# Performance work log

Measured on AMD Instinct MI355X. Metric: run time of the kernel, lower is better.

Reference implementation:

```python
import jax, jax.numpy as jnp
import numpy as np

N_NODES = 100000
N_EDGES = 1600000
NFEAT = 512
HIDDEN = 128
NCLASS = 40


def setup_inputs() -> dict:
    key = jax.random.key(0)
    ks = jax.random.split(key, 8)
    x = jax.random.normal(ks[0], (N_NODES, NFEAT), dtype=jnp.float32)
    edge_src = jax.random.randint(ks[1], (N_EDGES,), 0, N_NODES, dtype=jnp.int32)
    edge_dst = jax.random.randint(ks[2], (N_EDGES,), 0, N_NODES, dtype=jnp.int32)
    # normalized adjacency values (D^-1/2 A D^-1/2 style), all positive
    edge_val = jax.random.uniform(ks[3], (N_EDGES,), dtype=jnp.float32)
    # glorot-ish init like pygcn's reset_parameters
    W1 = jax.random.normal(ks[4], (NFEAT, HIDDEN), dtype=jnp.float32) / np.sqrt(NFEAT)
    b1 = jnp.zeros((HIDDEN,), dtype=jnp.float32)
    W2 = jax.random.normal(ks[5], (HIDDEN, NCLASS), dtype=jnp.float32) / np.sqrt(HIDDEN)
    b2 = jnp.zeros((NCLASS,), dtype=jnp.float32)
    return {"x": x, "edge_src": edge_src, "edge_dst": edge_dst, "edge_val": edge_val,
            "W1": W1, "b1": b1, "W2": W2, "b2": b2}


def _gcn_layer(h, edge_src, edge_dst, edge_val, W, b):
    # support = h @ W ; out = spmm(adj, support) + b
    support = h @ W                                  # [N, d_out]
    msg = support[edge_src] * edge_val[:, None]      # [E, d_out] gather
    agg = jax.ops.segment_sum(msg, edge_dst, num_segments=N_NODES)  # scatter-add
    return agg + b


def reference(x, edge_src, edge_dst, edge_val, W1, b1, W2, b2):
    h = _gcn_layer(x, edge_src, edge_dst, edge_val, W1, b1)
    h = jax.nn.relu(h)
    # dropout=0.0 -> branch skipped (faithful to `if self.dropout:` with falsy value)
    h = _gcn_layer(h, edge_src, edge_dst, edge_val, W2, b2)
    return jax.nn.log_softmax(h, axis=1)
```

## Files before the change

kernel.cpp:

```cpp
#include <hip/hip_runtime.h>
#include <stdint.h>

#define NN 100000
#define NE 1600000
#define NF 512
#define NH 128
#define NC 40
#define BKT 64
#define DEGS 16
#define NGB 782

typedef float f32x4 __attribute__((ext_vector_type(4)));
typedef short bf16x8 __attribute__((ext_vector_type(8)));

__device__ __forceinline__ unsigned short f2bf(float f){
    unsigned u = __float_as_uint(f);
    u = u + 0x7FFFu + ((u >> 16) & 1u);
    return (unsigned short)(u >> 16);
}
__device__ __forceinline__ unsigned pk2(float a, float b){
    return (unsigned)f2bf(a) | ((unsigned)f2bf(b) << 16);
}
__device__ __forceinline__ float blo(unsigned u){ return __uint_as_float(u << 16); }
__device__ __forceinline__ float bhi(unsigned u){ return __uint_as_float(u & 0xffff0000u); }

__global__ __launch_bounds__(256) void wprep(const float* __restrict__ W1, const float* __restrict__ W2,
                                             unsigned short* __restrict__ W1t, unsigned short* __restrict__ W2t){
    int tid = blockIdx.x * 256 + threadIdx.x;
    if (tid < NF * NH){
        int c = tid >> 9;
        int k = tid & 511;
        W1t[c * NF + k] = f2bf(W1[k * NH + c]);
    }
    int t2 = tid - NF * NH;
    if (t2 >= 0 && t2 < 48 * NH){
        int c = t2 >> 7;
        int k = t2 & 127;
        W2t[c * NH + k] = (c < NC) ? f2bf(W2[k * NC + c]) : (unsigned short)0;
    }
}

__global__ __launch_bounds__(256, 3) void gemm1_edge(const float* __restrict__ x,
                                                     const unsigned short* __restrict__ W1t,
                                                     unsigned short* __restrict__ s1,
                                                     const int* __restrict__ esrc,
                                                     const int* __restrict__ edst,
                                                     const float* __restrict__ eval,
                                                     int* __restrict__ deg, int2* __restrict__ pk){
    __shared__ unsigned short Al[2][128 * 40];
    __shared__ unsigned short Bl[2][128 * 40];
    if (blockIdx.x >= NGB){
        int tid = (blockIdx.x - NGB) * 256 + threadIdx.x;
        if (tid < NE){
            int d = edst[tid];
            int pos = atomicAdd(&deg[d * DEGS], 1);
            if (pos < BKT)
                pk[(size_t)d * BKT + pos] = make_int2(esrc[tid], __float_as_int(eval[tid]));
        }
        return;
    }
    const int tid  = threadIdx.x;
    const int wid  = tid >> 6;
    const int lane = tid & 63;
    const int quad = lane >> 4;
    const int l15  = lane & 15;
    const int br   = blockIdx.x * 128;

    const int r    = tid >> 1;
    const int half = tid & 1;

    int arow = br + r; if (arow >= NN) arow = NN - 1;
    const float* aptr = x + (size_t)arow * NF + half * 16;
    const unsigned short* bptr = W1t + (size_t)r * NF + half * 16;

    float4 pa0, pa1, pa2, pa3;
    uint4  pb0, pb1;
    {
        const float4* ap = (const float4*)aptr;
        pa0 = ap[0]; pa1 = ap[1]; pa2 = ap[2]; pa3 = ap[3];
        const uint4* bp = (const uint4*)bptr;
        pb0 = bp[0]; pb1 = bp[1];
        unsigned* Ad = (unsigned*)&Al[0][r * 40 + half * 16];
        Ad[0] = pk2(pa0.x, pa0.y); Ad[1] = pk2(pa0.z, pa0.w);
        Ad[2] = pk2(pa1.x, pa1.y); Ad[3] = pk2(pa1.z, pa1.w);
        Ad[4] = pk2(pa2.x, pa2.y); Ad[5] = pk2(pa2.z, pa2.w);
        Ad[6] = pk2(pa3.x, pa3.y); Ad[7] = pk2(pa3.z, pa3.w);
        uint4* Bd = (uint4*)&Bl[0][r * 40 + half * 16];
        Bd[0] = pb0; Bd[1] = pb1;
    }
    __syncthreads();

    f32x4 acc[2][8];
#pragma unroll
    for (int i = 0; i < 2; i++)
#pragma unroll
        for (int j = 0; j < 8; j++) acc[i][j] = (f32x4){0.f, 0.f, 0.f, 0.f};

    int cur = 0;
    for (int ks = 0; ks < NF; ks += 32){
        const bool more = (ks + 32 < NF);
        if (more){
            const float4* ap = (const float4*)(aptr + ks + 32);
            pa0 = ap[0]; pa1 = ap[1]; pa2 = ap[2]; pa3 = ap[3];
            const uint4* bp = (const uint4*)(bptr + ks + 32);
            pb0 = bp[0]; pb1 = bp[1];
        }

        bf16x8 a0 = *(const bf16x8*)&Al[cur][(wid * 32 +      l15) * 40 + quad * 8];
        bf16x8 a1 = *(const bf16x8*)&Al[cur][(wid * 32 + 16 + l15) * 40 + quad * 8];
        bf16x8 bb[8];
#pragma unroll
        for (int ct = 0; ct < 8; ct++)
            bb[ct] = *(const bf16x8*)&Bl[cur][(ct * 16 + l15) * 40 + quad * 8];
#pragma unroll
        for (int ct = 0; ct < 8; ct++){
            acc[0][ct] = __builtin_amdgcn_mfma_f32_16x16x32_bf16(a0, bb[ct], acc[0][ct], 0, 0, 0);
            acc[1][ct] = __builtin_amdgcn_mfma_f32_16x16x32_bf16(a1, bb[ct], acc[1][ct], 0, 0, 0);
        }

        if (more){
            int nxt = cur ^ 1;
            unsigned* Ad = (unsigned*)&Al[nxt][r * 40 + half * 16];
            Ad[0] = pk2(pa0.x, pa0.y); Ad[1] = pk2(pa0.z, pa0.w);
            Ad[2] = pk2(pa1.x, pa1.y); Ad[3] = pk2(pa1.z, pa1.w);
            Ad[4] = pk2(pa2.x, pa2.y); Ad[5] = pk2(pa2.z, pa2.w);
            Ad[6] = pk2(pa3.x, pa3.y); Ad[7] = pk2(pa3.z, pa3.w);
            uint4* Bd = (uint4*)&Bl[nxt][r * 40 + half * 16];
            Bd[0] = pb0; Bd[1] = pb1;
        }
        __syncthreads();
        cur ^= 1;
    }

#pragma unroll
    for (int rt = 0; rt < 2; rt++)
#pragma unroll
        for (int ct = 0; ct < 8; ct++)
#pragma unroll
            for (int i = 0; i < 4; i++){
                int row = br + wid * 32 + rt * 16 + quad * 4 + i;
                if (row < NN) s1[(size_t)row * NH + ct * 16 + l15] = f2bf(acc[rt][ct][i]);
            }
}

__global__ __launch_bounds__(256) void agg1g2(const uint4* __restrict__ s1v,
                                              const int* __restrict__ deg,
                                              const int2* __restrict__ pk,
                                              const float* __restrict__ b1,
                                              const unsigned short* __restrict__ W2t,
                                              unsigned short* __restrict__ s2p){
    __shared__ unsigned short Hl[64][136];
    const int tid   = threadIdx.x;
    const int wid   = tid >> 6;
    const int lane  = tid & 63;
    const int quad  = lane >> 4;
    const int hl    = lane & 15;
    const int lbase = quad * 16;
    const int nb    = blockIdx.x * 64;

    const float4* b1v = (const float4*)b1;
    const float4 bA = b1v[2 * hl], bB = b1v[2 * hl + 1];

#pragma unroll
    for (int pass = 0; pass < 4; pass++){
        const int nloc = pass * 16 + wid * 4 + quad;
        const int node = nb + nloc;
        float a[8];
#pragma unroll
        for (int t = 0; t < 8; t++) a[t] = 0.f;

        if (node < NN){
            const int s = node * BKT;
            int dg = deg[node * DEGS]; if (dg > BKT) dg = BKT;
            const int e = s + dg;

            int2 rec = make_int2(0, 0);
            {
                int c0 = e - s; if (c0 > 16) c0 = 16;
                if (hl < c0) rec = pk[s + hl];
            }
            for (int base = s; base < e; base += 16){
                int cnt = e - base; if (cnt > 16) cnt = 16;
                int2 cur = rec;
                int nxb = base + 16;
                if (nxb < e){
                    int cn = e - nxb; if (cn > 16) cn = 16;
                    rec = make_int2(0, 0);
                    if (hl < cn) rec = pk[nxb + hl];
                }
                int j = 0;
                for (; j + 8 <= cnt; j += 8){
                    int is[8];
#pragma unroll
                    for (int q = 0; q < 8; q++) is[q] = __shfl(cur.x, lbase + j + q, 64);
                    uint4 us[8];
#pragma unroll
                    for (int q = 0; q < 8; q++) us[q] = s1v[(size_t)is[q] * 16 + hl];
                    float vs[8];
#pragma unroll
                    for (int q = 0; q < 8; q++) vs[q] = __int_as_float(__shfl(cur.y, lbase + j + q, 64));
#pragma unroll
                    for (int q = 0; q < 8; q++){
                        float v = vs[q];
                        a[0] += v * blo(us[q].x); a[1] += v * bhi(us[q].x);
                        a[2] += v * blo(us[q].y); a[3] += v * bhi(us[q].y);
                        a[4] += v * blo(us[q].z); a[5] += v * bhi(us[q].z);
                        a[6] += v * blo(us[q].w); a[7] += v * bhi(us[q].w);
                    }
                }
                for (; j < cnt; j++){
                    int   i0 = __shfl(cur.x, lbase + j, 64);
                    float v0 = __int_as_float(__shfl(cur.y, lbase + j, 64));
                    uint4 u  = s1v[(size_t)i0 * 16 + hl];
                    a[0] += v0 * blo(u.x); a[1] += v0 * bhi(u.x);
                    a[2] += v0 * blo(u.y); a[3] += v0 * bhi(u.y);
                    a[4] += v0 * blo(u.z); a[5] += v0 * bhi(u.z);
                    a[6] += v0 * blo(u.w); a[7] += v0 * bhi(u.w);
                }
            }
            a[0] += bA.x; a[1] += bA.y; a[2] += bA.z; a[3] += bA.w;
            a[4] += bB.x; a[5] += bB.y; a[6] += bB.z; a[7] += bB.w;
#pragma unroll
            for (int t = 0; t < 8; t++) a[t] = fmaxf(a[t], 0.f);
        }
        *(uint4*)&Hl[nloc][hl * 8] = make_uint4(pk2(a[0], a[1]), pk2(a[2], a[3]),
                                                pk2(a[4], a[5]), pk2(a[6], a[7]));
    }
    __syncthreads();

    bf16x8 bf[3][4];
#pragma unroll
    for (int ct = 0; ct < 3; ct++)
#pragma unroll
        for (int ks = 0; ks < 4; ks++)
            bf[ct][ks] = *(const bf16x8*)&W2t[(ct * 16 + hl) * NH + ks * 32 + quad * 8];

    bf16x8 af[4];
#pragma unroll
    for (int ks = 0; ks < 4; ks++)
        af[ks] = *(const bf16x8*)&Hl[wid * 16 + hl][ks * 32 + quad * 8];

    f32x4 acc[3];
#pragma unroll
    for (int ct = 0; ct < 3; ct++) acc[ct] = (f32x4){0.f, 0.f, 0.f, 0.f};
#pragma unroll
    for (int ks = 0; ks < 4; ks++)
#pragma unroll
        for (int ct = 0; ct < 3; ct++)
            acc[ct] = __builtin_amdgcn_mfma_f32_16x16x32_bf16(af[ks], bf[ct][ks], acc[ct], 0, 0, 0);

#pragma unroll
    for (int ct = 0; ct < 3; ct++)
#pragma unroll
        for (int i = 0; i < 4; i++){
            int row = nb + wid * 16 + quad * 4 + i;
            if (row < NN) s2p[(size_t)row * 64 + ct * 16 + hl] = f2bf(acc[ct][i]);
        }
}

__global__ __launch_bounds__(256) void agg2(const uint4* __restrict__ s2v,
                                            const int* __restrict__ deg,
                                            const int2* __restrict__ pk,
                                            const float* __restrict__ b2, float* __restrict__ out){
    const int lane  = threadIdx.x & 63;
    const int oct   = lane >> 3;
    const int hl    = lane & 7;
    const int lbase = oct * 8;
    const int node  = blockIdx.x * 32 + (threadIdx.x >> 6) * 8 + oct;

    const int s = node * BKT;
    int dg = deg[node * DEGS]; if (dg > BKT) dg = BKT;
    const int e = s + dg;
    float a[8];
#pragma unroll
    for (int t = 0; t < 8; t++) a[t] = 0.f;

    int2 rec = make_int2(0, 0);
    {
        int c0 = e - s; if (c0 > 8) c0 = 8;
        if (hl < c0) rec = pk[s + hl];
    }
    for (int base = s; base < e; base += 8){
        int cnt = e - base; if (cnt > 8) cnt = 8;
        int2 cur = rec;
        int nb = base + 8;
        if (nb < e){
            int cn = e - nb; if (cn > 8) cn = 8;
            rec = make_int2(0, 0);
            if (hl < cn) rec = pk[nb + hl];
        }
        if (cnt == 8){
            int is[8];
#pragma unroll
            for (int q = 0; q < 8; q++) is[q] = __shfl(cur.x, lbase + q, 64);
            uint4 us[8];
#pragma unroll
            for (int q = 0; q < 8; q++) us[q] = s2v[(size_t)is[q] * 8 + hl];
            float vs[8];
#pragma unroll
            for (int q = 0; q < 8; q++) vs[q] = __int_as_float(__shfl(cur.y, lbase + q, 64));
#pragma unroll
            for (int q = 0; q < 8; q++){
                float v = vs[q];
                a[0] += v * blo(us[q].x); a[1] += v * bhi(us[q].x);
                a[2] += v * blo(us[q].y); a[3] += v * bhi(us[q].y);
                a[4] += v * blo(us[q].z); a[5] += v * bhi(us[q].z);
                a[6] += v * blo(us[q].w); a[7] += v * bhi(us[q].w);
            }
        } else {
            for (int j = 0; j < cnt; j++){
                int   i0 = __shfl(cur.x, lbase + j, 64);
                float v0 = __int_as_float(__shfl(cur.y, lbase + j, 64));
                uint4 u  = s2v[(size_t)i0 * 8 + hl];
                a[0] += v0 * blo(u.x); a[1] += v0 * bhi(u.x);
                a[2] += v0 * blo(u.y); a[3] += v0 * bhi(u.y);
                a[4] += v0 * blo(u.z); a[5] += v0 * bhi(u.z);
                a[6] += v0 * blo(u.w); a[7] += v0 * bhi(u.w);
            }
        }
    }
    const bool act = hl < 5;
    float z[8];
    if (act){
        const float4* b2v = (const float4*)b2;
        float4 cA = b2v[2 * hl], cB = b2v[2 * hl + 1];
        z[0] = a[0] + cA.x; z[1] = a[1] + cA.y; z[2] = a[2] + cA.z; z[3] = a[3] + cA.w;
        z[4] = a[4] + cB.x; z[5] = a[5] + cB.y; z[6] = a[6] + cB.z; z[7] = a[7] + cB.w;
    } else {
#pragma unroll
        for (int t = 0; t < 8; t++) z[t] = -INFINITY;
    }
    float m = z[0];
#pragma unroll
    for (int t = 1; t < 8; t++) m = fmaxf(m, z[t]);
#pragma unroll
    for (int o = 4; o; o >>= 1) m = fmaxf(m, __shfl_xor(m, o, 8));
    float pe = 0.f;
    if (act){
#pragma unroll
        for (int t = 0; t < 8; t++) pe += __expf(z[t] - m);
    }
#pragma unroll
    for (int o = 4; o; o >>= 1) pe += __shfl_xor(pe, o, 8);
    if (act){
        float l = __logf(pe) + m;
        float* op = out + (size_t)node * NC + 8 * hl;
        *(float4*)op       = make_float4(z[0] - l, z[1] - l, z[2] - l, z[3] - l);
        *(float4*)(op + 4) = make_float4(z[4] - l, z[5] - l, z[6] - l, z[7] - l);
    }
}

extern "C" void kernel_launch(void* const* d_in, const int* in_sizes, int n_in,
                              void* d_out, int out_size, void* d_ws, size_t ws_size,
                              hipStream_t stream) {
    const float* x    = (const float*)d_in[0];
    const int*   esrc = (const int*)  d_in[1];
    const int*   edst = (const int*)  d_in[2];
    const float* eval = (const float*)d_in[3];
    const float* W1   = (const float*)d_in[4];
    const float* b1   = (const float*)d_in[5];
    const float* W2   = (const float*)d_in[6];
    const float* b2   = (const float*)d_in[7];
    float* out = (float*)d_out;

    char* ws = (char*)d_ws;
    size_t off = 0;
    auto alloc = [&](size_t bytes) -> void* {
        void* p = ws + off;
        off += (bytes + 255) & ~(size_t)255;
        return p;
    };
    unsigned short* W1t  = (unsigned short*)alloc((size_t)NF * NH * 2);
    unsigned short* W2t  = (unsigned short*)alloc((size_t)48 * NH * 2);
    unsigned short* s1   = (unsigned short*)alloc((size_t)NN * NH * 2);
    unsigned short* s2p  = (unsigned short*)alloc((size_t)NN * 64 * 2);
    int*   deg   = (int*)  alloc((size_t)NN * DEGS * 4);
    int2*  pk    = (int2*) alloc((size_t)NN * BKT * 8);

    hipMemsetAsync(deg, 0, (size_t)NN * DEGS * 4, stream);

    wprep     <<<280, 256, 0, stream>>>(W1, W2, W1t, W2t);
    gemm1_edge<<<NGB + (NE + 255) / 256, 256, 0, stream>>>(x, W1t, s1, esrc, edst, eval, deg, pk);
    agg1g2    <<<(NN + 63) / 64, 256, 0, stream>>>((const uint4*)s1, deg, pk, b1, W2t, s2p);
    agg2      <<<NN / 32, 256, 0, stream>>>((const uint4*)s2p, deg, pk, b2, out);
}
```

Measured before the change: 505.7 us.

## Pack edge src and bf16 value into one word with inline degree counter

```diff
diff --git a/kernel.cpp b/kernel.cpp
--- a/kernel.cpp
+++ b/kernel.cpp
@@ -6,8 +6,6 @@
 #define NF 512
 #define NH 128
 #define NC 40
-#define BKT 64
-#define DEGS 16
 #define NGB 782
 
 typedef float f32x4 __attribute__((ext_vector_type(4)));
@@ -23,6 +21,8 @@
 }
 __device__ __forceinline__ float blo(unsigned u){ return __uint_as_float(u << 16); }
 __device__ __forceinline__ float bhi(unsigned u){ return __uint_as_float(u & 0xffff0000u); }
+__device__ __forceinline__ float pval(unsigned p){ return __uint_as_float((p & 0x7fffu) << 16); }
+__device__ __forceinline__ unsigned psrc(unsigned p){ return p >> 15; }
 
 __global__ __launch_bounds__(256) void wprep(const float* __restrict__ W1, const float* __restrict__ W2,
                                              unsigned short* __restrict__ W1t, unsigned short* __restrict__ W2t){
@@ -46,16 +46,17 @@
                                                      const int* __restrict__ esrc,
                                                      const int* __restrict__ edst,
                                                      const float* __restrict__ eval,
-                                                     int* __restrict__ deg, int2* __restrict__ pk){
+                                                     unsigned* __restrict__ pkc){
     __shared__ unsigned short Al[2][128 * 40];
     __shared__ unsigned short Bl[2][128 * 40];
     if (blockIdx.x >= NGB){
         int tid = (blockIdx.x - NGB) * 256 + threadIdx.x;
         if (tid < NE){
             int d = edst[tid];
-            int pos = atomicAdd(&deg[d * DEGS], 1);
-            if (pos < BKT)
-                pk[(size_t)d * BKT + pos] = make_int2(esrc[tid], __float_as_int(eval[tid]));
+            unsigned pv = ((unsigned)esrc[tid] << 15) | ((unsigned)f2bf(eval[tid]) & 0x7fffu);
+            unsigned pos = atomicAdd(&pkc[(size_t)d * 64], 1u);
+            if (pos < 63u)
+                pkc[(size_t)d * 64 + 1 + pos] = pv;
         }
         return;
     }
@@ -144,8 +145,7 @@
 }
 
 __global__ __launch_bounds__(256) void agg1g2(const uint4* __restrict__ s1v,
-                                              const int* __restrict__ deg,
-                                              const int2* __restrict__ pk,
+                                              const unsigned* __restrict__ pkc,
                                               const float* __restrict__ b1,
                                               const unsigned short* __restrict__ W2t,
                                               unsigned short* __restrict__ s2p){
@@ -170,38 +170,45 @@
         for (int t = 0; t < 8; t++) a[t] = 0.f;
 
         if (node < NN){
-            const int s = node * BKT;
-            int dg = deg[node * DEGS]; if (dg > BKT) dg = BKT;
-            const int e = s + dg;
-
-            int2 rec = make_int2(0, 0);
-            {
-                int c0 = e - s; if (c0 > 16) c0 = 16;
-                if (hl < c0) rec = pk[s + hl];
-            }
-            for (int base = s; base < e; base += 16){
-                int cnt = e - base; if (cnt > 16) cnt = 16;
-                int2 cur = rec;
-                int nxb = base + 16;
-                if (nxb < e){
-                    int cn = e - nxb; if (cn > 16) cn = 16;
-                    rec = make_int2(0, 0);
-                    if (hl < cn) rec = pk[nxb + hl];
-                }
+            const unsigned sbase = (unsigned)node * 64;
+            unsigned rec = pkc[sbase + hl];
+            unsigned cntw = __shfl(rec, lbase, 64);
+            int dg = (cntw > 63u) ? 63 : (int)cntw;
+            int done = 0, lskip = 1;
+            unsigned sb = sbase;
+            while (done < dg){
+                int cnt = dg - done;
+                int room = 16 - lskip; if (cnt > room) cnt = room;
+                unsigned curc = rec;
+                unsigned nsb = sb + 16;
+                if (done + cnt < dg) rec = pkc[nsb + hl];
                 int j = 0;
                 for (; j + 8 <= cnt; j += 8){
-                    int is[8];
-#pragma unroll
-                    for (int q = 0; q < 8; q++) is[q] = __shfl(cur.x, lbase + j + q, 64);
+                    unsigned ps[8];
+#pragma unroll
+                    for (int q = 0; q < 8; q++) ps[q] = __shfl(curc, lbase + lskip + j + q, 64);
                     uint4 us[8];
 #pragma unroll
-                    for (int q = 0; q < 8; q++) us[q] = s1v[(size_t)is[q] * 16 + hl];
-                    float vs[8];
-#pragma unroll
-                    for (int q = 0; q < 8; q++) vs[q] = __int_as_float(__shfl(cur.y, lbase + j + q, 64));
+                    for (int q = 0; q < 8; q++) us[q] = s1v[(size_t)psrc(ps[q]) * 16 + hl];
 #pragma unroll
                     for (int q = 0; q < 8; q++){
-                        float v = vs[q];
+                        float v = pval(ps[q]);
+                        a[0] += v * blo(us[q].x); a[1] += v * bhi(us[q].x);
+                        a[2] += v * blo(us[q].y); a[3] += v * bhi(us[q].y);
+                        a[4] += v * blo(us[q].z); a[5] += v * bhi(us[q].z);
+                        a[6] += v * blo(us[q].w); a[7] += v * bhi(us[q].w);
+                    }
+                }
+                for (; j + 4 <= cnt; j += 4){
+                    unsigned ps[4];
+#pragma unroll
+                    for (int q = 0; q < 4; q++) ps[q] = __shfl(curc, lbase + lskip + j + q, 64);
+                    uint4 us[4];
+#pragma unroll
+                    for (int q = 0; q < 4; q++) us[q] = s1v[(size_t)psrc(ps[q]) * 16 + hl];
+#pragma unroll
+                    for (int q = 0; q < 4; q++){
+                        float v = pval(ps[q]);
                         a[0] += v * blo(us[q].x); a[1] += v * bhi(us[q].x);
                         a[2] += v * blo(us[q].y); a[3] += v * bhi(us[q].y);
                         a[4] += v * blo(us[q].z); a[5] += v * bhi(us[q].z);
@@ -209,14 +216,15 @@
                     }
                 }
                 for (; j < cnt; j++){
-                    int   i0 = __shfl(cur.x, lbase + j, 64);
-                    float v0 = __int_as_float(__shfl(cur.y, lbase + j, 64));
-                    uint4 u  = s1v[(size_t)i0 * 16 + hl];
-                    a[0] += v0 * blo(u.x); a[1] += v0 * bhi(u.x);
-                    a[2] += v0 * blo(u.y); a[3] += v0 * bhi(u.y);
-                    a[4] += v0 * blo(u.z); a[5] += v0 * bhi(u.z);
-                    a[6] += v0 * blo(u.w); a[7] += v0 * bhi(u.w);
+                    unsigned p = __shfl(curc, lbase + lskip + j, 64);
+                    float v = pval(p);
+                    uint4 u  = s1v[(size_t)psrc(p) * 16 + hl];
+                    a[0] += v * blo(u.x); a[1] += v * bhi(u.x);
+                    a[2] += v * blo(u.y); a[3] += v * bhi(u.y);
+                    a[4] += v * blo(u.z); a[5] += v * bhi(u.z);
+                    a[6] += v * blo(u.w); a[7] += v * bhi(u.w);
                 }
+                done += cnt; sb = nsb; lskip = 0;
             }
             a[0] += bA.x; a[1] += bA.y; a[2] += bA.z; a[3] += bA.w;
             a[4] += bB.x; a[5] += bB.y; a[6] += bB.z; a[7] += bB.w;
@@ -259,8 +267,7 @@
 }
 
 __global__ __launch_bounds__(256) void agg2(const uint4* __restrict__ s2v,
-                                            const int* __restrict__ deg,
-                                            const int2* __restrict__ pk,
+                                            const unsigned* __restrict__ pkc,
                                             const float* __restrict__ b2, float* __restrict__ out){
     const int lane  = threadIdx.x & 63;
     const int oct   = lane >> 3;
@@ -268,56 +275,49 @@
     const int lbase = oct * 8;
     const int node  = blockIdx.x * 32 + (threadIdx.x >> 6) * 8 + oct;
 
-    const int s = node * BKT;
-    int dg = deg[node * DEGS]; if (dg > BKT) dg = BKT;
-    const int e = s + dg;
     float a[8];
 #pragma unroll
     for (int t = 0; t < 8; t++) a[t] = 0.f;
 
-    int2 rec = make_int2(0, 0);
-    {
-        int c0 = e - s; if (c0 > 8) c0 = 8;
-        if (hl < c0) rec = pk[s + hl];
-    }
-    for (int base = s; base < e; base += 8){
-        int cnt = e - base; if (cnt > 8) cnt = 8;
-        int2 cur = rec;
-        int nb = base + 8;
-        if (nb < e){
-            int cn = e - nb; if (cn > 8) cn = 8;
-            rec = make_int2(0, 0);
-            if (hl < cn) rec = pk[nb + hl];
-        }
-        if (cnt == 8){
-            int is[8];
-#pragma unroll
-            for (int q = 0; q < 8; q++) is[q] = __shfl(cur.x, lbase + q, 64);
-            uint4 us[8];
-#pragma unroll
-            for (int q = 0; q < 8; q++) us[q] = s2v[(size_t)is[q] * 8 + hl];
-            float vs[8];
-#pragma unroll
-            for (int q = 0; q < 8; q++) vs[q] = __int_as_float(__shfl(cur.y, lbase + q, 64));
-#pragma unroll
-            for (int q = 0; q < 8; q++){
-                float v = vs[q];
+    const unsigned sbase = (unsigned)node * 64;
+    unsigned rec = pkc[sbase + hl];
+    unsigned cntw = __shfl(rec, lbase, 64);
+    int dg = (cntw > 63u) ? 63 : (int)cntw;
+    int done = 0, lskip = 1;
+    unsigned sb = sbase;
+    while (done < dg){
+        int cnt = dg - done;
+        int room = 8 - lskip; if (cnt > room) cnt = room;
+        unsigned curc = rec;
+        unsigned nsb = sb + 8;
+        if (done + cnt < dg) rec = pkc[nsb + hl];
+        int j = 0;
+        for (; j + 4 <= cnt; j += 4){
+            unsigned ps[4];
+#pragma unroll
+            for (int q = 0; q < 4; q++) ps[q] = __shfl(curc, lbase + lskip + j + q, 64);
+            uint4 us[4];
+#pragma unroll
+            for (int q = 0; q < 4; q++) us[q] = s2v[(size_t)psrc(ps[q]) * 8 + hl];
+#pragma unroll
+            for (int q = 0; q < 4; q++){
+                float v = pval(ps[q]);
                 a[0] += v * blo(us[q].x); a[1] += v * bhi(us[q].x);
                 a[2] += v * blo(us[q].y); a[3] += v * bhi(us[q].y);
                 a[4] += v * blo(us[q].z); a[5] += v * bhi(us[q].z);
                 a[6] += v * blo(us[q].w); a[7] += v * bhi(us[q].w);
             }
-        } else {
-            for (int j = 0; j < cnt; j++){
-                int   i0 = __shfl(cur.x, lbase + j, 64);
-                float v0 = __int_as_float(__shfl(cur.y, lbase + j, 64));
-                uint4 u  = s2v[(size_t)i0 * 8 + hl];
-                a[0] += v0 * blo(u.x); a[1] += v0 * bhi(u.x);
-                a[2] += v0 * blo(u.y); a[3] += v0 * bhi(u.y);
-                a[4] += v0 * blo(u.z); a[5] += v0 * bhi(u.z);
-                a[6] += v0 * blo(u.w); a[7] += v0 * bhi(u.w);
-            }
-        }
+        }
+        for (; j < cnt; j++){
+            unsigned p = __shfl(curc, lbase + lskip + j, 64);
+            float v = pval(p);
+            uint4 u  = s2v[(size_t)psrc(p) * 8 + hl];
+            a[0] += v * blo(u.x); a[1] += v * bhi(u.x);
+            a[2] += v * blo(u.y); a[3] += v * bhi(u.y);
+            a[4] += v * blo(u.z); a[5] += v * bhi(u.z);
+            a[6] += v * blo(u.w); a[7] += v * bhi(u.w);
+        }
+        done += cnt; sb = nsb; lskip = 0;
     }
     const bool act = hl < 5;
     float z[8];
@@ -334,14 +334,14 @@
 #pragma unroll
     for (int t = 1; t < 8; t++) m = fmaxf(m, z[t]);
 #pragma unroll
-    for (int o = 4; o; o >>= 1) m = fmaxf(m, __shfl_xor(m, o, 8));
+    for (int o = 4; o; o >>= 1) m = fmaxf(m, __shfl_xor(m, o, 64));
     float pe = 0.f;
     if (act){
 #pragma unroll
         for (int t = 0; t < 8; t++) pe += __expf(z[t] - m);
     }
 #pragma unroll
-    for (int o = 4; o; o >>= 1) pe += __shfl_xor(pe, o, 8);
+    for (int o = 4; o; o >>= 1) pe += __shfl_xor(pe, o, 64);
     if (act){
         float l = __logf(pe) + m;
         float* op = out + (size_t)node * NC + 8 * hl;
@@ -374,13 +374,12 @@
     unsigned short* W2t  = (unsigned short*)alloc((size_t)48 * NH * 2);
     unsigned short* s1   = (unsigned short*)alloc((size_t)NN * NH * 2);
     unsigned short* s2p  = (unsigned short*)alloc((size_t)NN * 64 * 2);
-    int*   deg   = (int*)  alloc((size_t)NN * DEGS * 4);
-    int2*  pk    = (int2*) alloc((size_t)NN * BKT * 8);
-
-    hipMemsetAsync(deg, 0, (size_t)NN * DEGS * 4, stream);
+    unsigned*       pkc  = (unsigned*)     alloc((size_t)NN * 64 * 4);
+
+    hipMemsetAsync(pkc, 0, (size_t)NN * 64 * 4, stream);
 
     wprep     <<<280, 256, 0, stream>>>(W1, W2, W1t, W2t);
-    gemm1_edge<<<NGB + (NE + 255) / 256, 256, 0, stream>>>(x, W1t, s1, esrc, edst, eval, deg, pk);
-    agg1g2    <<<(NN + 63) / 64, 256, 0, stream>>>((const uint4*)s1, deg, pk, b1, W2t, s2p);
-    agg2      <<<NN / 32, 256, 0, stream>>>((const uint4*)s2p, deg, pk, b2, out);
-}
+    gemm1_edge<<<NGB + (NE + 255) / 256, 256, 0, stream>>>(x, W1t, s1, esrc, edst, eval, pkc);
+    agg1g2    <<<(NN + 63) / 64, 256, 0, stream>>>((const uint4*)s1, pkc, b1, W2t, s2p);
+    agg2      <<<NN / 32, 256, 0, stream>>>((const uint4*)s2p, pkc, b2, out);
+}
```

Result: no change. 511.7 us (+1.2%).
